# Performance work log

Measured on AMD Instinct MI355X. Metric: run time of the kernel, lower is better.

Reference implementation:

```python
import jax, jax.numpy as jnp
import numpy as np

NUM_TAGS = 128
NUM_FEATURES = 500000
B, T, F = 64, 512, 8


def setup_inputs() -> dict:
    key = jax.random.key(0)
    ks = jax.random.split(key, 6)
    feats = jax.random.randint(ks[0], (B, T, F), 0, NUM_FEATURES)
    tags = jax.random.randint(ks[1], (B, T), 0, NUM_TAGS)
    # original init: uniform(-0.01, 0.01)
    state_weights = jax.random.uniform(ks[2], (NUM_TAGS, NUM_FEATURES), minval=-0.01, maxval=0.01, dtype=jnp.float32)
    transitions = jax.random.uniform(ks[3], (NUM_TAGS, NUM_TAGS), minval=-0.01, maxval=0.01, dtype=jnp.float32)
    start_transitions = jax.random.uniform(ks[4], (NUM_TAGS,), minval=-0.01, maxval=0.01, dtype=jnp.float32)
    end_transitions = jax.random.uniform(ks[5], (NUM_TAGS,), minval=-0.01, maxval=0.01, dtype=jnp.float32)
    return dict(feats=feats, tags=tags, state_weights=state_weights,
                transitions=transitions, start_transitions=start_transitions,
                end_transitions=end_transitions)


def reference(feats, tags, state_weights, transitions, start_transitions, end_transitions):
    """Batched CRF negative log-likelihood per sentence: logZ - gold_score. Returns [B]."""
    # emissions[b,t,k] = sum_f state_weights[k, feats[b,t,f]]  (emissions_for_sentence)
    emissions = jnp.take(state_weights, feats, axis=1).sum(-1)   # [K,B,T]
    emissions = jnp.moveaxis(emissions, 0, -1)                    # [B,T,K]

    # log_partition: forward algorithm over T via scan
    alpha0 = start_transitions[None, :] + emissions[:, 0]         # [B,K]

    def step(alpha, em_t):
        # scores[b,i,j] = alpha[b,i] + transitions[i,j]
        scores = alpha[:, :, None] + transitions[None, :, :]
        return jax.nn.logsumexp(scores, axis=1) + em_t, None

    em_rest = jnp.moveaxis(emissions[:, 1:], 1, 0)                # [T-1,B,K]
    alphaT, _ = jax.lax.scan(step, alpha0, em_rest)
    log_z = jax.nn.logsumexp(alphaT + end_transitions[None, :], axis=1)   # [B]

    # gold_score, vectorized over batch
    em_gold = jnp.take_along_axis(emissions, tags[..., None], axis=2)[..., 0].sum(axis=1)  # [B]
    trans_gold = transitions[tags[:, :-1], tags[:, 1:]].sum(axis=1)                        # [B]
    gold = start_transitions[tags[:, 0]] + end_transitions[tags[:, -1]] + em_gold + trans_gold

    return log_z - gold
```

## Files before the change

kernel.cpp:

```cpp
#include <hip/hip_runtime.h>

#define NUM_TAGS 128
#define NUM_FEATS 500000
#define BB 64
#define TT 512
#define FF 8

#define SWT_BYTES 256000000ull
#define EM_BYTES  16777216ull
#define NEED_FULL (SWT_BYTES + EM_BYTES)

typedef float f2 __attribute__((ext_vector_type(2)));

#define AP(j) ((((j) >> 5) * 36) + ((j) & 31))

__device__ __forceinline__ void barrier_lds() {
  asm volatile("s_waitcnt lgkmcnt(0)" ::: "memory");
  __builtin_amdgcn_s_barrier();
  __builtin_amdgcn_sched_barrier(0);
}

__global__ __launch_bounds__(256) void transpose_kernel(
    const float* __restrict__ sw, float* __restrict__ swT) {
  __shared__ float tile[32][129];
  const int f0 = blockIdx.x * 32;
  const int t = threadIdx.x;
  const int fi = t & 31, kb = t >> 5;
#pragma unroll
  for (int it = 0; it < 16; ++it) {
    int k = kb + it * 8;
    tile[fi][k] = sw[(size_t)k * NUM_FEATS + f0 + fi];
  }
  __syncthreads();
  const int k2 = t & 127, fo = t >> 7;
#pragma unroll
  for (int it = 0; it < 16; ++it) {
    int f2i = fo + it * 2;
    swT[(size_t)(f0 + f2i) * NUM_TAGS + k2] = tile[f2i][k2];
  }
}

__global__ __launch_bounds__(128) void gather_t_kernel(
    const int* __restrict__ feats, const float* __restrict__ swT,
    float* __restrict__ em_exp) {
  const int token = blockIdx.x;
  const int k = threadIdx.x;
  const int* f = feats + token * FF;
  float s = 0.f;
#pragma unroll
  for (int i = 0; i < FF; ++i) s += swT[(size_t)f[i] * NUM_TAGS + k];
  em_exp[(size_t)token * NUM_TAGS + k] = __expf(s);
}

__global__ __launch_bounds__(128) void gather_f_kernel(
    const int* __restrict__ feats, const float* __restrict__ sw,
    float* __restrict__ em_exp) {
  const int token = blockIdx.x;
  const int k = threadIdx.x;
  const int* f = feats + token * FF;
  const float* row = sw + (size_t)k * NUM_FEATS;
  float s = 0.f;
#pragma unroll
  for (int i = 0; i < FF; ++i) s += row[f[i]];
  em_exp[(size_t)token * NUM_TAGS + k] = __expf(s);
}

__device__ __forceinline__ void stepv(float& evreg, int t,
                                      const float* __restrict__ embx,
                                      int j, int q, const float* alf_src,
                                      float* alf_dst, const f2 (&eTv)[16]) {
  float ev = evreg;
  int tp = t + 4; if (tp > TT - 1) tp = TT - 1;
  evreg = embx[tp * NUM_TAGS + j];
  const float4* a4 = (const float4*)(alf_src + q * 36);
  f2 acc0 = {0.f, 0.f}, acc1 = {0.f, 0.f};
#pragma unroll
  for (int i = 0; i < 8; ++i) {
    float4 a = a4[i];
    acc0 += (f2){a.x, a.y} * eTv[2 * i];
    acc1 += (f2){a.z, a.w} * eTv[2 * i + 1];
  }
  float r = (acc0.x + acc0.y) + (acc1.x + acc1.y);
  r += __shfl_xor(r, 1, 64);
  r += __shfl_xor(r, 2, 64);
  if (q == 0) alf_dst[AP(j)] = r * ev * 0.0078125f;
  barrier_lds();
}

__global__ __launch_bounds__(512, 1) void fwd_kernel(
    const float* __restrict__ em_exp, const int* __restrict__ tags,
    const float* __restrict__ trans, const float* __restrict__ startT,
    const float* __restrict__ endT, float* __restrict__ out) {
  const int b = blockIdx.x;
  const int tid = threadIdx.x;
  const int j = tid >> 2, q = tid & 3;

  __shared__ __align__(16) float alf[2][144];
  __shared__ float sred[16];

  f2 eTv[16];
#pragma unroll
  for (int i = 0; i < 16; ++i) {
    eTv[i].x = __expf(trans[(32 * q + 2 * i) * NUM_TAGS + j]);
    eTv[i].y = __expf(trans[(32 * q + 2 * i + 1) * NUM_TAGS + j]);
  }

  const float* embx = em_exp + (size_t)b * TT * NUM_TAGS;

  if (q == 0) alf[0][AP(j)] = __expf(startT[j]) * embx[j];

  float evA = embx[1 * NUM_TAGS + j], evB = embx[2 * NUM_TAGS + j],
        evC = embx[3 * NUM_TAGS + j], evD = embx[4 * NUM_TAGS + j];
  __syncthreads();

  int cur = 0;
  for (int t = 1; t + 3 < TT; t += 4) {
    stepv(evA, t + 0, embx, j, q, alf[cur], alf[cur ^ 1], eTv); cur ^= 1;
    stepv(evB, t + 1, embx, j, q, alf[cur], alf[cur ^ 1], eTv); cur ^= 1;
    stepv(evC, t + 2, embx, j, q, alf[cur], alf[cur ^ 1], eTv); cur ^= 1;
    stepv(evD, t + 3, embx, j, q, alf[cur], alf[cur ^ 1], eTv); cur ^= 1;
  }
  stepv(evA, 509, embx, j, q, alf[cur], alf[cur ^ 1], eTv); cur ^= 1;
  stepv(evB, 510, embx, j, q, alf[cur], alf[cur ^ 1], eTv); cur ^= 1;
  stepv(evC, 511, embx, j, q, alf[cur], alf[cur ^ 1], eTv); cur ^= 1;

  if (tid < 128) {
    float val = alf[cur][AP(tid)] * __expf(endT[tid]);
#pragma unroll
    for (int off = 32; off > 0; off >>= 1) val += __shfl_down(val, off, 64);
    if ((tid & 63) == 0) sred[tid >> 6] = val;
  }

  const int* tb = tags + b * TT;
  const int t = tid;
  const int tg = tb[t];
  float g = __logf(embx[t * NUM_TAGS + tg]);
  if (t < TT - 1) g += trans[tg * NUM_TAGS + tb[t + 1]];
  if (t == 0) g += startT[tb[0]] + endT[tb[TT - 1]];
#pragma unroll
  for (int off = 32; off > 0; off >>= 1) g += __shfl_down(g, off, 64);
  if ((tid & 63) == 0) sred[8 + (tid >> 6)] = g;
  __syncthreads();

  if (tid == 0) {
    float logz = __logf(sred[0] + sred[1]) + 511.0f * 7.0f * 0.69314718055994531f;
    float gs = 0.f;
#pragma unroll
    for (int i = 0; i < 8; ++i) gs += sred[8 + i];
    out[b] = logz - gs;
  }
}

extern "C" void kernel_launch(void* const* d_in, const int* in_sizes, int n_in,
                              void* d_out, int out_size, void* d_ws, size_t ws_size,
                              hipStream_t stream) {
  const int* feats = (const int*)d_in[0];
  const int* tags = (const int*)d_in[1];
  const float* sw = (const float*)d_in[2];
  const float* trans = (const float*)d_in[3];
  const float* startT = (const float*)d_in[4];
  const float* endT = (const float*)d_in[5];
  float* out = (float*)d_out;

  if (ws_size >= NEED_FULL) {
    float* swT = (float*)d_ws;
    float* em_exp = (float*)((char*)d_ws + SWT_BYTES);
    transpose_kernel<<<NUM_FEATS / 32, 256, 0, stream>>>(sw, swT);
    gather_t_kernel<<<BB * TT, 128, 0, stream>>>(feats, swT, em_exp);
    fwd_kernel<<<BB, 512, 0, stream>>>(em_exp, tags, trans, startT, endT, out);
  } else {
    float* em_exp = (float*)d_ws;
    gather_f_kernel<<<BB * TT, 128, 0, stream>>>(feats, sw, em_exp);
    fwd_kernel<<<BB, 512, 0, stream>>>(em_exp, tags, trans, startT, endT, out);
  }
}
```

Before: 565.4 us.

## Use one thread per tag in forward recursion, dropping shuffle reduction

The forward-algorithm kernel changes from 4 threads per output tag (512 threads with cross-lane shuffles) to one thread per tag (128 threads), each holding all 128 exp-transition values in registers. This removes the two shuffle steps per timestep and makes the barrier cover only 2 waves instead of 8. The cost is 4x more FMA and LDS-read work per thread on the serial critical path, plus much higher register pressure. The gold-score loop is adjusted so each thread covers 4 timesteps.

```diff
diff --git a/kernel.cpp b/kernel.cpp
--- a/kernel.cpp
+++ b/kernel.cpp
@@ -11,8 +11,6 @@
 #define NEED_FULL (SWT_BYTES + EM_BYTES)
 
 typedef float f2 __attribute__((ext_vector_type(2)));
-
-#define AP(j) ((((j) >> 5) * 36) + ((j) & 31))
 
 __device__ __forceinline__ void barrier_lds() {
   asm volatile("s_waitcnt lgkmcnt(0)" ::: "memory");
@@ -65,89 +63,92 @@
   em_exp[(size_t)token * NUM_TAGS + k] = __expf(s);
 }
 
-__device__ __forceinline__ void stepv(float& evreg, int t,
-                                      const float* __restrict__ embx,
-                                      int j, int q, const float* alf_src,
-                                      float* alf_dst, const f2 (&eTv)[16]) {
+__device__ __forceinline__ void stepw(float& evreg, int t,
+                                      const float* __restrict__ embx, int j,
+                                      const float* alf_src, float* alf_dst,
+                                      const f2 (&eT2)[64]) {
   float ev = evreg;
   int tp = t + 4; if (tp > TT - 1) tp = TT - 1;
   evreg = embx[tp * NUM_TAGS + j];
-  const float4* a4 = (const float4*)(alf_src + q * 36);
-  f2 acc0 = {0.f, 0.f}, acc1 = {0.f, 0.f};
+  const float4* a4 = (const float4*)alf_src;
+  f2 acc0 = {0.f, 0.f}, acc1 = {0.f, 0.f}, acc2 = {0.f, 0.f}, acc3 = {0.f, 0.f};
 #pragma unroll
   for (int i = 0; i < 8; ++i) {
-    float4 a = a4[i];
-    acc0 += (f2){a.x, a.y} * eTv[2 * i];
-    acc1 += (f2){a.z, a.w} * eTv[2 * i + 1];
+    float4 a = a4[4 * i + 0], b = a4[4 * i + 1];
+    float4 c = a4[4 * i + 2], d = a4[4 * i + 3];
+    acc0 += (f2){a.x, a.y} * eT2[8 * i + 0];
+    acc1 += (f2){a.z, a.w} * eT2[8 * i + 1];
+    acc2 += (f2){b.x, b.y} * eT2[8 * i + 2];
+    acc3 += (f2){b.z, b.w} * eT2[8 * i + 3];
+    acc0 += (f2){c.x, c.y} * eT2[8 * i + 4];
+    acc1 += (f2){c.z, c.w} * eT2[8 * i + 5];
+    acc2 += (f2){d.x, d.y} * eT2[8 * i + 6];
+    acc3 += (f2){d.z, d.w} * eT2[8 * i + 7];
   }
-  float r = (acc0.x + acc0.y) + (acc1.x + acc1.y);
-  r += __shfl_xor(r, 1, 64);
-  r += __shfl_xor(r, 2, 64);
-  if (q == 0) alf_dst[AP(j)] = r * ev * 0.0078125f;
+  f2 sA = acc0 + acc1, sB = acc2 + acc3;
+  f2 sC = sA + sB;
+  alf_dst[j] = (sC.x + sC.y) * ev * 0.0078125f;
   barrier_lds();
 }
 
-__global__ __launch_bounds__(512, 1) void fwd_kernel(
+__global__ __launch_bounds__(128, 1) void fwd_kernel(
     const float* __restrict__ em_exp, const int* __restrict__ tags,
     const float* __restrict__ trans, const float* __restrict__ startT,
     const float* __restrict__ endT, float* __restrict__ out) {
   const int b = blockIdx.x;
-  const int tid = threadIdx.x;
-  const int j = tid >> 2, q = tid & 3;
+  const int j = threadIdx.x;
 
-  __shared__ __align__(16) float alf[2][144];
-  __shared__ float sred[16];
+  __shared__ __align__(16) float alf[2][NUM_TAGS];
+  __shared__ float sred[4];
 
-  f2 eTv[16];
+  f2 eT2[64];
 #pragma unroll
-  for (int i = 0; i < 16; ++i) {
-    eTv[i].x = __expf(trans[(32 * q + 2 * i) * NUM_TAGS + j]);
-    eTv[i].y = __expf(trans[(32 * q + 2 * i + 1) * NUM_TAGS + j]);
+  for (int m = 0; m < 64; ++m) {
+    eT2[m].x = __expf(trans[(2 * m) * NUM_TAGS + j]);
+    eT2[m].y = __expf(trans[(2 * m + 1) * NUM_TAGS + j]);
   }
 
   const float* embx = em_exp + (size_t)b * TT * NUM_TAGS;
 
-  if (q == 0) alf[0][AP(j)] = __expf(startT[j]) * embx[j];
-
+  alf[0][j] = __expf(startT[j]) * embx[j];
   float evA = embx[1 * NUM_TAGS + j], evB = embx[2 * NUM_TAGS + j],
         evC = embx[3 * NUM_TAGS + j], evD = embx[4 * NUM_TAGS + j];
   __syncthreads();
 
   int cur = 0;
   for (int t = 1; t + 3 < TT; t += 4) {
-    stepv(evA, t + 0, embx, j, q, alf[cur], alf[cur ^ 1], eTv); cur ^= 1;
-    stepv(evB, t + 1, embx, j, q, alf[cur], alf[cur ^ 1], eTv); cur ^= 1;
-    stepv(evC, t + 2, embx, j, q, alf[cur], alf[cur ^ 1], eTv); cur ^= 1;
-    stepv(evD, t + 3, embx, j, q, alf[cur], alf[cur ^ 1], eTv); cur ^= 1;
+    stepw(evA, t + 0, embx, j, alf[cur], alf[cur ^ 1], eT2); cur ^= 1;
+    stepw(evB, t + 1, embx, j, alf[cur], alf[cur ^ 1], eT2); cur ^= 1;
+    stepw(evC, t + 2, embx, j, alf[cur], alf[cur ^ 1], eT2); cur ^= 1;
+    stepw(evD, t + 3, embx, j, alf[cur], alf[cur ^ 1], eT2); cur ^= 1;
   }
-  stepv(evA, 509, embx, j, q, alf[cur], alf[cur ^ 1], eTv); cur ^= 1;
-  stepv(evB, 510, embx, j, q, alf[cur], alf[cur ^ 1], eTv); cur ^= 1;
-  stepv(evC, 511, embx, j, q, alf[cur], alf[cur ^ 1], eTv); cur ^= 1;
+  stepw(evA, 509, embx, j, alf[cur], alf[cur ^ 1], eT2); cur ^= 1;
+  stepw(evB, 510, embx, j, alf[cur], alf[cur ^ 1], eT2); cur ^= 1;
+  stepw(evC, 511, embx, j, alf[cur], alf[cur ^ 1], eT2); cur ^= 1;
 
-  if (tid < 128) {
-    float val = alf[cur][AP(tid)] * __expf(endT[tid]);
+  float val = alf[cur][j] * __expf(endT[j]);
 #pragma unroll
-    for (int off = 32; off > 0; off >>= 1) val += __shfl_down(val, off, 64);
-    if ((tid & 63) == 0) sred[tid >> 6] = val;
-  }
+  for (int off = 32; off > 0; off >>= 1) val += __shfl_down(val, off, 64);
+  if ((j & 63) == 0) sred[j >> 6] = val;
 
   const int* tb = tags + b * TT;
-  const int t = tid;
-  const int tg = tb[t];
-  float g = __logf(embx[t * NUM_TAGS + tg]);
-  if (t < TT - 1) g += trans[tg * NUM_TAGS + tb[t + 1]];
-  if (t == 0) g += startT[tb[0]] + endT[tb[TT - 1]];
+  float g = 0.f;
+#pragma unroll
+  for (int p = 0; p < 4; ++p) {
+    int t = j + 128 * p;
+    int tg = tb[t];
+    g += __logf(embx[t * NUM_TAGS + tg]);
+    if (t < TT - 1) g += trans[tg * NUM_TAGS + tb[t + 1]];
+  }
+  if (j == 0) g += startT[tb[0]] + endT[tb[TT - 1]];
 #pragma unroll
   for (int off = 32; off > 0; off >>= 1) g += __shfl_down(g, off, 64);
-  if ((tid & 63) == 0) sred[8 + (tid >> 6)] = g;
+  if ((j & 63) == 0) sred[2 + (j >> 6)] = g;
   __syncthreads();
 
-  if (tid == 0) {
+  if (j == 0) {
     float logz = __logf(sred[0] + sred[1]) + 511.0f * 7.0f * 0.69314718055994531f;
-    float gs = 0.f;
-#pragma unroll
-    for (int i = 0; i < 8; ++i) gs += sred[8 + i];
-    out[b] = logz - gs;
+    out[b] = logz - (sred[2] + sred[3]);
   }
 }
 
@@ -167,10 +168,10 @@
     float* em_exp = (float*)((char*)d_ws + SWT_BYTES);
     transpose_kernel<<<NUM_FEATS / 32, 256, 0, stream>>>(sw, swT);
     gather_t_kernel<<<BB * TT, 128, 0, stream>>>(feats, swT, em_exp);
-    fwd_kernel<<<BB, 512, 0, stream>>>(em_exp, tags, trans, startT, endT, out);
+    fwd_kernel<<<BB, 128, 0, stream>>>(em_exp, tags, trans, startT, endT, out);
   } else {
     float* em_exp = (float*)d_ws;
     gather_f_kernel<<<BB * TT, 128, 0, stream>>>(feats, sw, em_exp);
-    fwd_kernel<<<BB, 512, 0, stream>>>(em_exp, tags, trans, startT, endT, out);
+    fwd_kernel<<<BB, 128, 0, stream>>>(em_exp, tags, trans, startT, endT, out);
   }
 }
```

Result: slower. 637.1 us (+12.7%).
